# Optimization experiments

Measured on AMD Instinct MI355X. Metric: run time of the kernel, lower is better.

Reference implementation:

```python
import jax, jax.numpy as jnp
import numpy as np

L, B, S, D, H, FF, V, P = 6, 8, 1024, 768, 12, 3072, 50257, 1024
DH = D // H
EPS = 1e-5


def setup_inputs() -> dict:
    key = jax.random.key(0)
    ks = jax.random.split(key, 12)
    std = 0.02
    return {
        "x_ids": jax.random.randint(ks[0], (B, S), 0, V),
        "calibrated_mask": jax.random.normal(ks[1], (B, S, S), jnp.float32),
        "wte": jax.random.normal(ks[2], (V, D), jnp.float32) * std,
        "wpe": jax.random.normal(ks[3], (P, D), jnp.float32) * std,
        "ln1_g": jnp.ones((L, D), jnp.float32),
        "ln1_b": jnp.zeros((L, D), jnp.float32),
        "qkv_w": jax.random.normal(ks[4], (L, D, 3 * D), jnp.float32) * std,
        "qkv_b": jnp.zeros((L, 3 * D), jnp.float32),
        "ao_w": jax.random.normal(ks[5], (L, D, D), jnp.float32) * std,
        "ao_b": jnp.zeros((L, D), jnp.float32),
        "ln2_g": jnp.ones((L, D), jnp.float32),
        "ln2_b": jnp.zeros((L, D), jnp.float32),
        "fc_w": jax.random.normal(ks[6], (L, D, FF), jnp.float32) * std,
        "fc_b": jnp.zeros((L, FF), jnp.float32),
        "op_w": jax.random.normal(ks[7], (L, FF, D), jnp.float32) * std,
        "op_b": jnp.zeros((L, D), jnp.float32),
        "lnf_g": jnp.ones((D,), jnp.float32),
        "lnf_b": jnp.zeros((D,), jnp.float32),
    }


def _ln(x, g, b):
    m = jnp.mean(x, axis=-1, keepdims=True)
    v = jnp.var(x, axis=-1, keepdims=True)
    return (x - m) * jax.lax.rsqrt(v + EPS) * g + b


def _gelu_new(x):
    c = np.sqrt(2.0 / np.pi).astype(np.float32)
    return 0.5 * x * (1.0 + jnp.tanh(c * (x + 0.044715 * x * x * x)))


def _gpt2_forward(x_ids, calibrated_mask, wte, wpe, ln1_g, ln1_b, qkv_w, qkv_b,
                  ao_w, ao_b, ln2_g, ln2_b, fc_w, fc_b, op_w, op_b, lnf_g, lnf_b):
    s = x_ids.shape[1]
    h = wte[x_ids] + wpe[:s][None, :, :]  # [B,S,D]
    causal = jnp.tril(jnp.ones((s, s), bool))
    neg = jnp.finfo(h.dtype).min
    # additive mask, broadcast over heads (unsqueeze(1).repeat over n_head)
    add_mask = calibrated_mask[:, None, :, :]  # [B,1,S,S]

    def block(hid, p):
        l1g, l1b, qw, qb, aw, ab, l2g, l2b, fw, fb, ow, ob = p
        x = _ln(hid, l1g, l1b)
        qkv = x @ qw + qb  # [B,S,3D]
        q, k, v = jnp.split(qkv, 3, axis=-1)
        q = q.reshape(q.shape[0], s, H, DH).transpose(0, 2, 1, 3)
        k = k.reshape(k.shape[0], s, H, DH).transpose(0, 2, 1, 3)
        v = v.reshape(v.shape[0], s, H, DH).transpose(0, 2, 1, 3)
        scores = jnp.einsum('bhqd,bhkd->bhqk', q, k) / jnp.sqrt(jnp.asarray(DH, q.dtype))
        scores = jnp.where(causal[None, None], scores, neg)
        scores = scores + add_mask
        w = jax.nn.softmax(scores, axis=-1)
        a = jnp.einsum('bhqk,bhkd->bhqd', w, v)
        a = a.transpose(0, 2, 1, 3).reshape(a.shape[0], s, D)
        hid = hid + a @ aw + ab
        x2 = _ln(hid, l2g, l2b)
        hid = hid + _gelu_new(x2 @ fw + fb) @ ow + ob
        return hid, None

    params = (ln1_g, ln1_b, qkv_w, qkv_b, ao_w, ao_b, ln2_g, ln2_b, fc_w, fc_b, op_w, op_b)
    h, _ = jax.lax.scan(block, h, params)
    return _ln(h, lnf_g, lnf_b)


def reference(x_ids, calibrated_mask, wte, wpe, ln1_g, ln1_b, qkv_w, qkv_b,
              ao_w, ao_b, ln2_g, ln2_b, fc_w, fc_b, op_w, op_b, lnf_g, lnf_b):
    return _gpt2_forward(x_ids, calibrated_mask, wte, wpe, ln1_g, ln1_b, qkv_w, qkv_b,
                         ao_w, ao_b, ln2_g, ln2_b, fc_w, fc_b, op_w, op_b, lnf_g, lnf_b)
```

## Files before the change

### kernel.cpp

```cpp
#include <hip/hip_runtime.h>
#include <hip/hip_bf16.h>

typedef __bf16 bf16_t;
typedef __bf16 bf16x8 __attribute__((ext_vector_type(8)));
typedef float  f32x4  __attribute__((ext_vector_type(4)));

#define DEV __device__ __forceinline__

DEV void gload_lds16(const void* g, void* l) {
  __builtin_amdgcn_global_load_lds(
      (__attribute__((address_space(1))) void*)(void*)g,
      (__attribute__((address_space(3))) void*)l, 16, 0, 0);
}

__global__ __launch_bounds__(256)
void transpose_cast(const float* __restrict__ in, bf16_t* __restrict__ out,
                    int K, int N) {
  __shared__ float tile[32][33];
  const int k0 = blockIdx.x * 32;
  const int n0 = blockIdx.y * 32;
  const int tx = threadIdx.x;
  const int ty = threadIdx.y;
#pragma unroll
  for (int i = 0; i < 32; i += 8)
    tile[ty + i][tx] = in[(long)(k0 + ty + i) * N + n0 + tx];
  __syncthreads();
#pragma unroll
  for (int i = 0; i < 32; i += 8)
    out[(long)(n0 + ty + i) * K + k0 + tx] = (bf16_t)tile[tx][ty + i];
}

__global__ __launch_bounds__(256)
void embed_kernel(const int* __restrict__ ids, const float* __restrict__ wte,
                  const float* __restrict__ wpe, bf16_t* __restrict__ h) {
  const int idx = blockIdx.x * 256 + threadIdx.x;
  const int col = idx % 768;
  const int row = idx / 768;
  const int s   = row & 1023;
  h[idx] = (bf16_t)(wte[(long)ids[row] * 768 + col] + wpe[s * 768 + col]);
}

template <bool BF16OUT>
__global__ __launch_bounds__(256)
void ln_kernel(const bf16_t* __restrict__ x, const float* __restrict__ g,
               const float* __restrict__ b, bf16_t* __restrict__ ob,
               float* __restrict__ of) {
  const long row = blockIdx.x;
  const bf16_t* xr = x + row * 768;
  const int t = threadIdx.x;
  float v0 = (float)xr[t], v1 = (float)xr[t + 256], v2 = (float)xr[t + 512];
  float s  = v0 + v1 + v2;
  float sq = v0 * v0 + v1 * v1 + v2 * v2;
#pragma unroll
  for (int o = 32; o; o >>= 1) { s += __shfl_down(s, o); sq += __shfl_down(sq, o); }
  __shared__ float red[8];
  const int w = t >> 6;
  if ((t & 63) == 0) { red[w] = s; red[4 + w] = sq; }
  __syncthreads();
  s  = red[0] + red[1] + red[2] + red[3];
  sq = red[4] + red[5] + red[6] + red[7];
  const float mean = s * (1.f / 768.f);
  const float rs = rsqrtf(sq * (1.f / 768.f) - mean * mean + 1e-5f);
  float vv[3] = {v0, v1, v2};
#pragma unroll
  for (int i = 0; i < 3; ++i) {
    const int col = t + i * 256;
    const float o2 = (vv[i] - mean) * rs * g[col] + b[col];
    if (BF16OUT) ob[row * 768 + col] = (bf16_t)o2;
    else         of[row * 768 + col] = o2;
  }
}

template <int EPI, int BN>
__global__ __launch_bounds__(256, 4)
void gemm_bt(const bf16_t* __restrict__ A, const bf16_t* __restrict__ Bt,
             const float* __restrict__ bias, bf16_t* __restrict__ Cb,
             int M, int N, int K) {
  constexpr int NI = BN / 32;
  __shared__ bf16_t As[128 * 64];
  __shared__ bf16_t Bs[BN * 64];
  const int tid  = threadIdx.x;
  const int lane = tid & 63, w = tid >> 6;
  const int col = lane & 15, s16 = lane >> 4;
  const int nbn = N / BN;
  const int cpx = gridDim.x >> 3;
  const int bid = (blockIdx.x & 7) * cpx + (blockIdx.x >> 3);
  const int bm = bid / nbn, bn = bid % nbn;
  const int wr = w >> 1, wc = w & 1;

  f32x4 acc[4][NI];
#pragma unroll
  for (int i = 0; i < 4; ++i)
#pragma unroll
    for (int j = 0; j < NI; ++j) acc[i][j] = f32x4{0.f, 0.f, 0.f, 0.f};

  const long arow0 = (long)bm * 128;
  const long brow0 = (long)bn * BN;

  const int nt = K >> 6;
  for (int t = 0; t < nt; ++t) {
    const int k0 = t << 6;
#pragma unroll
    for (int i = 0; i < 4; ++i) {
      const int c = i * 256 + tid;
      const int row = c >> 3, slot = c & 7;
      gload_lds16(A + (arow0 + row) * (long)K + k0 + ((slot ^ (row & 7)) << 3),
                  (char*)As + c * 16);
    }
#pragma unroll
    for (int i = 0; i < BN / 32; ++i) {
      const int c = i * 256 + tid;
      const int row = c >> 3, slot = c & 7;
      gload_lds16(Bt + (brow0 + row) * (long)K + k0 + ((slot ^ (row & 7)) << 3),
                  (char*)Bs + c * 16);
    }
    __syncthreads();

    bf16x8 af[2][4], bfr[2][NI];
#pragma unroll
    for (int mi = 0; mi < 4; ++mi) {
      const int row = wr * 64 + mi * 16 + col;
#pragma unroll
      for (int ks = 0; ks < 2; ++ks) {
        const int slot = ks * 4 + s16;
        af[ks][mi] = *(const bf16x8*)((char*)As + row * 128 +
                                      ((slot ^ (row & 7)) << 4));
      }
    }
#pragma unroll
    for (int ni = 0; ni < NI; ++ni) {
      const int row = wc * (BN / 2) + ni * 16 + col;
#pragma unroll
      for (int ks = 0; ks < 2; ++ks) {
        const int slot = ks * 4 + s16;
        bfr[ks][ni] = *(const bf16x8*)((char*)Bs + row * 128 +
                                       ((slot ^ (row & 7)) << 4));
      }
    }
#pragma unroll
    for (int ks = 0; ks < 2; ++ks)
#pragma unroll
      for (int mi = 0; mi < 4; ++mi)
#pragma unroll
        for (int ni = 0; ni < NI; ++ni)
          acc[mi][ni] = __builtin_amdgcn_mfma_f32_16x16x32_bf16(
              af[ks][mi], bfr[ks][ni], acc[mi][ni], 0, 0, 0);

    __syncthreads();
  }

  const int colb = bn * BN + wc * (BN / 2) + col;
  const int rowb = bm * 128 + wr * 64 + (s16 << 2);
#pragma unroll
  for (int ni = 0; ni < NI; ++ni) {
    const int ccol = colb + ni * 16;
    const float bv = bias[ccol];
#pragma unroll
    for (int mi = 0; mi < 4; ++mi) {
      const int row = rowb + mi * 16;
#pragma unroll
      for (int r = 0; r < 4; ++r) {
        const float v = acc[mi][ni][r] + bv;
        const long idx = (long)(row + r) * N + ccol;
        if (EPI == 1) {
          Cb[idx] = (bf16_t)((float)Cb[idx] + v);
        } else if (EPI == 2) {
          Cb[idx] = (bf16_t)v;
        } else {
          const float z = 0.7978845608028654f * (v + 0.044715f * v * v * v);
          Cb[idx] = (bf16_t)(v / (1.f + __expf(-2.f * z)));
        }
      }
    }
  }
}

__global__ __launch_bounds__(512, 4)
void gemm_wide(const bf16_t* __restrict__ A, const bf16_t* __restrict__ Bt,
               const float* __restrict__ bias, bf16_t* __restrict__ Cb,
               int M, int N, int K) {
  __shared__ bf16_t As[128 * 64];
  __shared__ bf16_t Bs[256 * 64];
  const int tid = threadIdx.x;
  const int lane = tid & 63, w = tid >> 6;
  const int col = lane & 15, s16 = lane >> 4;
  const int wm = w >> 2, wn = w & 3;
  const int nbn = N >> 8;
  const int cpx = gridDim.x >> 3;
  const int bid = (blockIdx.x & 7) * cpx + (blockIdx.x >> 3);
  const int bm = bid / nbn, bn = bid % nbn;
  const long arow0 = (long)bm * 128, brow0 = (long)bn * 256;

  f32x4 acc[4][4];
#pragma unroll
  for (int i = 0; i < 4; ++i)
#pragma unroll
    for (int j = 0; j < 4; ++j) acc[i][j] = f32x4{0.f, 0.f, 0.f, 0.f};

  const int nt = K >> 6;
  for (int t = 0; t < nt; ++t) {
    const int k0 = t << 6;
#pragma unroll
    for (int i = 0; i < 2; ++i) {
      const int c = i * 512 + tid;
      const int row = c >> 3, slot = c & 7;
      gload_lds16(A + (arow0 + row) * (long)K + k0 + ((slot ^ (row & 7)) << 3),
                  (char*)As + c * 16);
    }
#pragma unroll
    for (int i = 0; i < 4; ++i) {
      const int c = i * 512 + tid;
      const int row = c >> 3, slot = c & 7;
      gload_lds16(Bt + (brow0 + row) * (long)K + k0 + ((slot ^ (row & 7)) << 3),
                  (char*)Bs + c * 16);
    }
    __syncthreads();

    bf16x8 af[2][4], bfr[2][4];
#pragma unroll
    for (int mi = 0; mi < 4; ++mi) {
      const int row = wm * 64 + mi * 16 + col;
#pragma unroll
      for (int ks = 0; ks < 2; ++ks) {
        const int slot = ks * 4 + s16;
        af[ks][mi] = *(const bf16x8*)((char*)As + row * 128 +
                                      ((slot ^ (row & 7)) << 4));
      }
    }
#pragma unroll
    for (int ni = 0; ni < 4; ++ni) {
      const int row = wn * 64 + ni * 16 + col;
#pragma unroll
      for (int ks = 0; ks < 2; ++ks) {
        const int slot = ks * 4 + s16;
        bfr[ks][ni] = *(const bf16x8*)((char*)Bs + row * 128 +
                                       ((slot ^ (row & 7)) << 4));
      }
    }
#pragma unroll
    for (int ks = 0; ks < 2; ++ks)
#pragma unroll
      for (int mi = 0; mi < 4; ++mi)
#pragma unroll
        for (int ni = 0; ni < 4; ++ni)
          acc[mi][ni] = __builtin_amdgcn_mfma_f32_16x16x32_bf16(
              af[ks][mi], bfr[ks][ni], acc[mi][ni], 0, 0, 0);

    __syncthreads();
  }

  const int rowb = bm * 128 + wm * 64 + (s16 << 2);
  const int colb = bn * 256 + wn * 64 + col;
#pragma unroll
  for (int ni = 0; ni < 4; ++ni) {
    const int ccol = colb + ni * 16;
    const float bv = bias[ccol];
#pragma unroll
    for (int mi = 0; mi < 4; ++mi) {
      const int row = rowb + mi * 16;
#pragma unroll
      for (int r = 0; r < 4; ++r)
        Cb[(long)(row + r) * N + ccol] = (bf16_t)(acc[mi][ni][r] + bv);
    }
  }
}

__global__ __launch_bounds__(256, 3)
void attn_kernel(const bf16_t* __restrict__ qkv, const float* __restrict__ mask,
                 bf16_t* __restrict__ out) {
  __shared__ bf16_t Kl[2][64 * 64];
  __shared__ bf16_t Vt[2][64 * 64];
  __shared__ bf16_t Pl[4][16 * 64];
  const int tid = threadIdx.x, lane = tid & 63, w = tid >> 6;
  const int col = lane & 15, s16 = lane >> 4, l7 = lane & 7;
  const int qp = blockIdx.x & 7;
  const int bh = blockIdx.x >> 3;
  const int b = bh / 12, h = bh % 12;
  const int sw0 = (s16 ^ l7) << 4;
  const int sw1 = ((s16 + 4) ^ l7) << 4;
  char* const plw = (char*)&Pl[w][0];
  const long qkvb = (long)b * 1024 * 2304;

  auto stageK = [&](int buf, int k0) {
#pragma unroll
    for (int i = 0; i < 2; ++i) {
      const int c = i * 256 + tid;
      const int krow = c >> 3, slot = c & 7;
      gload_lds16(qkv + qkvb + (long)(k0 + krow) * 2304 + 768 + h * 64 +
                      ((slot ^ (krow & 7)) << 3),
                  (char*)&Kl[buf][0] + i * 4096 + w * 1024);
    }
  };
  auto loadV = [&](int k0, bf16x8& t0, bf16x8& t1) {
    const bf16_t* vbase = qkv + qkvb + 1536 + h * 64;
#pragma unroll
    for (int i = 0; i < 2; ++i) {
      const int c = i * 256 + tid;
      const int d = c & 63, koct = c >> 6;
      const bf16_t* vsrc = vbase + (long)(k0 + koct * 8) * 2304 + d;
      bf16x8 tv;
#pragma unroll
      for (int j = 0; j < 8; ++j) tv[j] = vsrc[(long)j * 2304];
      if (i == 0) t0 = tv; else t1 = tv;
    }
  };
  auto storeV = [&](int buf, const bf16x8& t0, const bf16x8& t1) {
#pragma unroll
    for (int i = 0; i < 2; ++i) {
      const int c = i * 256 + tid;
      const int d = c & 63, koct = c >> 6;
      *(bf16x8*)((char*)&Vt[buf][0] + d * 128 + ((koct ^ (d & 7)) << 4)) =
          (i == 0) ? t0 : t1;
    }
  };

#pragma unroll 1
  for (int pass = 0; pass < 2; ++pass) {
    const int qt = pass ? (15 - qp) : qp;
    const int qrow0 = qt * 64 + w * 16;
    const long rowQ = (long)(b * 1024 + qrow0 + col) * 2304 + h * 64;
    const bf16x8 aq0 = *(const bf16x8*)&qkv[rowQ + s16 * 8];
    const bf16x8 aq1 = *(const bf16x8*)&qkv[rowQ + 32 + s16 * 8];
    const int qb = qrow0 + s16 * 4;
    const float* mrow = mask + ((long)b * 1024 + qb) * 1024;

    auto loadM = [&](int k0, float (&m)[4][4]) {
#pragma unroll
      for (int g = 0; g < 4; ++g)
#pragma unroll
        for (int r = 0; r < 4; ++r)
          m[g][r] = mrow[(long)r * 1024 + k0 + g * 16 + col];
    };

    float m_run[4], l_run[4];
    f32x4 o_acc[4];
#pragma unroll
    for (int r = 0; r < 4; ++r) { m_run[r] = -INFINITY; l_run[r] = 0.f; }
#pragma unroll
    for (int go = 0; go < 4; ++go) o_acc[go] = f32x4{0.f, 0.f, 0.f, 0.f};

    bf16x8 tv0, tv1;
    stageK(0, 0);
    loadV(0, tv0, tv1);
    storeV(0, tv0, tv1);
    float msk[4][4];
    loadM(0, msk);
    __syncthreads();

#pragma unroll 1
    for (int kt = 0; kt <= qt; ++kt) {
      const int cur = kt & 1;
      const bool more = kt < qt;
      const int k0 = kt * 64;
      float mnx[4][4];
      if (more) {
        stageK(cur ^ 1, k0 + 64);
        loadV(k0 + 64, tv0, tv1);
        loadM(k0 + 64, mnx);
      }

      f32x4 sf[4];
      __builtin_amdgcn_s_setprio(1);
#pragma unroll
      for (int g = 0; g < 4; ++g) {
        const int rbyte = (g * 16 + col) * 128;
        bf16x8 bk0 = *(const bf16x8*)((char*)&Kl[cur][0] + rbyte + sw0);
        bf16x8 bk1 = *(const bf16x8*)((char*)&Kl[cur][0] + rbyte + sw1);
        f32x4 z = f32x4{0.f, 0.f, 0.f, 0.f};
        z = __builtin_amdgcn_mfma_f32_16x16x32_bf16(aq0, bk0, z, 0, 0, 0);
        z = __builtin_amdgcn_mfma_f32_16x16x32_bf16(aq1, bk1, z, 0, 0, 0);
        sf[g] = z;
      }
      __builtin_amdgcn_s_setprio(0);

      const bool diag = (kt == qt);
      float sv[4][4];
#pragma unroll
      for (int g = 0; g < 4; ++g)
#pragma unroll
        for (int r = 0; r < 4; ++r) {
          float s = sf[g][r] * 0.125f + msk[g][r];
          if (diag && (k0 + g * 16 + col) > (qb + r)) s = -INFINITY;
          sv[g][r] = s;
        }
#pragma unroll
      for (int r = 0; r < 4; ++r) {
        float mx = fmaxf(fmaxf(sv[0][r], sv[1][r]), fmaxf(sv[2][r], sv[3][r]));
#pragma unroll
        for (int o = 8; o; o >>= 1) mx = fmaxf(mx, __shfl_xor(mx, o));
        const float m_new = fmaxf(m_run[r], mx);
        const float f = __expf(m_run[r] - m_new);
        m_run[r] = m_new;
        float sum = 0.f;
#pragma unroll
        for (int g = 0; g < 4; ++g) {
          const float p = __expf(sv[g][r] - m_new);
          sv[g][r] = p;
          sum += p;
        }
#pragma unroll
        for (int o = 8; o; o >>= 1) sum += __shfl_xor(sum, o);
        l_run[r] = l_run[r] * f + sum;
#pragma unroll
        for (int go = 0; go < 4; ++go) o_acc[go][r] *= f;
      }

#pragma unroll
      for (int g = 0; g < 4; ++g) {
        const int ks = 2 * g + (col >> 3);
#pragma unroll
        for (int r = 0; r < 4; ++r) {
          const int qr = s16 * 4 + r;
          *(bf16_t*)(plw + qr * 128 + ((ks ^ (qr & 7)) << 4) + l7 * 2) = (bf16_t)sv[g][r];
        }
      }
      const bf16x8 pa0 = *(const bf16x8*)(plw + col * 128 + sw0);
      const bf16x8 pa1 = *(const bf16x8*)(plw + col * 128 + sw1);
      __builtin_amdgcn_s_setprio(1);
#pragma unroll
      for (int go = 0; go < 4; ++go) {
        const int dbyte = (go * 16 + col) * 128;
        bf16x8 bv0 = *(const bf16x8*)((char*)&Vt[cur][0] + dbyte + sw0);
        bf16x8 bv1 = *(const bf16x8*)((char*)&Vt[cur][0] + dbyte + sw1);
        o_acc[go] = __builtin_amdgcn_mfma_f32_16x16x32_bf16(pa0, bv0, o_acc[go], 0, 0, 0);
        o_acc[go] = __builtin_amdgcn_mfma_f32_16x16x32_bf16(pa1, bv1, o_acc[go], 0, 0, 0);
      }
      __builtin_amdgcn_s_setprio(0);

      if (more) {
        storeV(cur ^ 1, tv0, tv1);
#pragma unroll
        for (int g = 0; g < 4; ++g)
#pragma unroll
          for (int r = 0; r < 4; ++r) msk[g][r] = mnx[g][r];
      }
      __syncthreads();
    }

    float inv[4];
#pragma unroll
    for (int r = 0; r < 4; ++r) inv[r] = 1.f / l_run[r];
#pragma unroll
    for (int go = 0; go < 4; ++go)
#pragma unroll
      for (int r = 0; r < 4; ++r)
        out[(long)(b * 1024 + qb + r) * 768 + h * 64 + go * 16 + col] =
            (bf16_t)(o_acc[go][r] * inv[r]);
  }
}

extern "C" void kernel_launch(void* const* d_in, const int* in_sizes, int n_in,
                              void* d_out, int out_size, void* d_ws, size_t ws_size,
                              hipStream_t stream) {
  const int*   x_ids = (const int*)d_in[0];
  const float* mask  = (const float*)d_in[1];
  const float* wte   = (const float*)d_in[2];
  const float* wpe   = (const float*)d_in[3];
  const float* ln1_g = (const float*)d_in[4];
  const float* ln1_b = (const float*)d_in[5];
  const float* qkv_w = (const float*)d_in[6];
  const float* qkv_b = (const float*)d_in[7];
  const float* ao_w  = (const float*)d_in[8];
  const float* ao_b  = (const float*)d_in[9];
  const float* ln2_g = (const float*)d_in[10];
  const float* ln2_b = (const float*)d_in[11];
  const float* fc_w  = (const float*)d_in[12];
  const float* fc_b  = (const float*)d_in[13];
  const float* op_w  = (const float*)d_in[14];
  const float* op_b  = (const float*)d_in[15];
  const float* lnf_g = (const float*)d_in[16];
  const float* lnf_b = (const float*)d_in[17];

  char* ws = (char*)d_ws;
  size_t off = 0;
  auto alloc = [&](size_t bytes) {
    char* p = ws + off;
    off += (bytes + 255) & ~(size_t)255;
    return p;
  };
  bf16_t* wqT = (bf16_t*)alloc(6ull * 2304 * 768 * 2);
  bf16_t* waT = (bf16_t*)alloc(6ull * 768 * 768 * 2);
  bf16_t* wfT = (bf16_t*)alloc(6ull * 3072 * 768 * 2);
  bf16_t* woT = (bf16_t*)alloc(6ull * 768 * 3072 * 2);
  bf16_t* h   = (bf16_t*)alloc(8192ull * 768 * 2);
  bf16_t* xb  = (bf16_t*)alloc(8192ull * 768 * 2);
  bf16_t* qkv = (bf16_t*)alloc(8192ull * 2304 * 2);
  bf16_t* abf = (bf16_t*)alloc(8192ull * 768 * 2);
  bf16_t* fb  = (bf16_t*)alloc(8192ull * 3072 * 2);
  if (off > ws_size) return;

  const dim3 tb(32, 8);
  for (int l = 0; l < 6; ++l) {
    transpose_cast<<<dim3(768 / 32, 2304 / 32), tb, 0, stream>>>(
        qkv_w + (long)l * 768 * 2304, wqT + (long)l * 2304 * 768, 768, 2304);
    transpose_cast<<<dim3(768 / 32, 768 / 32), tb, 0, stream>>>(
        ao_w + (long)l * 768 * 768, waT + (long)l * 768 * 768, 768, 768);
    transpose_cast<<<dim3(768 / 32, 3072 / 32), tb, 0, stream>>>(
        fc_w + (long)l * 768 * 3072, wfT + (long)l * 3072 * 768, 768, 3072);
    transpose_cast<<<dim3(3072 / 32, 768 / 32), tb, 0, stream>>>(
        op_w + (long)l * 3072 * 768, woT + (long)l * 768 * 3072, 3072, 768);
  }

  embed_kernel<<<24576, 256, 0, stream>>>(x_ids, wte, wpe, h);

  for (int l = 0; l < 6; ++l) {
    ln_kernel<true><<<8192, 256, 0, stream>>>(h, ln1_g + l * 768, ln1_b + l * 768, xb, nullptr);
    gemm_wide<<<576, 512, 0, stream>>>(xb, wqT + (long)l * 2304 * 768,
                                       qkv_b + l * 2304, qkv, 8192, 2304, 768);
    attn_kernel<<<768, 256, 0, stream>>>(qkv, mask, abf);
    gemm_bt<1, 64><<<768, 256, 0, stream>>>(abf, waT + (long)l * 768 * 768,
                                            ao_b + l * 768, h, 8192, 768, 768);
    ln_kernel<true><<<8192, 256, 0, stream>>>(h, ln2_g + l * 768, ln2_b + l * 768, xb, nullptr);
    gemm_bt<3, 128><<<1536, 256, 0, stream>>>(xb, wfT + (long)l * 3072 * 768,
                                              fc_b + l * 3072, fb, 8192, 3072, 768);
    gemm_bt<1, 64><<<768, 256, 0, stream>>>(fb, woT + (long)l * 768 * 3072,
                                            op_b + l * 768, h, 8192, 768, 3072);
  }

  ln_kernel<false><<<8192, 256, 0, stream>>>(h, lnf_g, lnf_b, nullptr, (float*)d_out);
}
```

Measured before the change: 1.652 ms.

## Batch weight transposes, vectorize embed/LN, retile wide GEMM for QKV and FC

Collapses the 24 per-layer weight transpose launches into 4 launches using a z-grid dimension. Vectorizes the embedding kernel to 8 elements per thread and rewrites layernorm as one wavefront per row with xor-shuffle reduction, removing the shared-memory barrier. Retiles the 512-thread wide GEMM from 128x256 to 256x128 and templates its epilogue so the FC+GELU GEMM also uses it instead of the 256-thread kernel. These target launch overhead, scalar memory traffic and GEMM efficiency, at the risk of different occupancy and tile-quantization behaviour.

```diff
diff --git a/kernel.cpp b/kernel.cpp
--- a/kernel.cpp
+++ b/kernel.cpp
@@ -3,6 +3,7 @@
 
 typedef __bf16 bf16_t;
 typedef __bf16 bf16x8 __attribute__((ext_vector_type(8)));
+typedef __bf16 bf16x4 __attribute__((ext_vector_type(4)));
 typedef float  f32x4  __attribute__((ext_vector_type(4)));
 
 #define DEV __device__ __forceinline__
@@ -17,27 +18,35 @@
 void transpose_cast(const float* __restrict__ in, bf16_t* __restrict__ out,
                     int K, int N) {
   __shared__ float tile[32][33];
+  const long z = blockIdx.z;
+  const float* inz = in + z * (long)K * N;
+  bf16_t* outz = out + z * (long)N * K;
   const int k0 = blockIdx.x * 32;
   const int n0 = blockIdx.y * 32;
   const int tx = threadIdx.x;
   const int ty = threadIdx.y;
 #pragma unroll
   for (int i = 0; i < 32; i += 8)
-    tile[ty + i][tx] = in[(long)(k0 + ty + i) * N + n0 + tx];
+    tile[ty + i][tx] = inz[(long)(k0 + ty + i) * N + n0 + tx];
   __syncthreads();
 #pragma unroll
   for (int i = 0; i < 32; i += 8)
-    out[(long)(n0 + ty + i) * K + k0 + tx] = (bf16_t)tile[tx][ty + i];
+    outz[(long)(n0 + ty + i) * K + k0 + tx] = (bf16_t)tile[tx][ty + i];
 }
 
 __global__ __launch_bounds__(256)
 void embed_kernel(const int* __restrict__ ids, const float* __restrict__ wte,
                   const float* __restrict__ wpe, bf16_t* __restrict__ h) {
-  const int idx = blockIdx.x * 256 + threadIdx.x;
-  const int col = idx % 768;
-  const int row = idx / 768;
+  const int t = blockIdx.x * 256 + threadIdx.x;
+  const int row = t / 96;
+  const int c8  = (t % 96) * 8;
   const int s   = row & 1023;
-  h[idx] = (bf16_t)(wte[(long)ids[row] * 768 + col] + wpe[s * 768 + col]);
+  const float* wr = wte + (long)ids[row] * 768 + c8;
+  const float* pr = wpe + (long)s * 768 + c8;
+  bf16x8 o;
+#pragma unroll
+  for (int j = 0; j < 8; ++j) o[j] = (bf16_t)(wr[j] + pr[j]);
+  *(bf16x8*)&h[(long)row * 768 + c8] = o;
 }
 
 template <bool BF16OUT>
@@ -45,29 +54,48 @@
 void ln_kernel(const bf16_t* __restrict__ x, const float* __restrict__ g,
                const float* __restrict__ b, bf16_t* __restrict__ ob,
                float* __restrict__ of) {
-  const long row = blockIdx.x;
+  const int lane = threadIdx.x & 63;
+  const long row = blockIdx.x * 4 + (threadIdx.x >> 6);
   const bf16_t* xr = x + row * 768;
-  const int t = threadIdx.x;
-  float v0 = (float)xr[t], v1 = (float)xr[t + 256], v2 = (float)xr[t + 512];
-  float s  = v0 + v1 + v2;
-  float sq = v0 * v0 + v1 * v1 + v2 * v2;
-#pragma unroll
-  for (int o = 32; o; o >>= 1) { s += __shfl_down(s, o); sq += __shfl_down(sq, o); }
-  __shared__ float red[8];
-  const int w = t >> 6;
-  if ((t & 63) == 0) { red[w] = s; red[4 + w] = sq; }
-  __syncthreads();
-  s  = red[0] + red[1] + red[2] + red[3];
-  sq = red[4] + red[5] + red[6] + red[7];
+  const bf16x8 v8 = *(const bf16x8*)&xr[lane * 8];
+  const bf16x4 v4 = *(const bf16x4*)&xr[512 + lane * 4];
+  float vv[12];
+#pragma unroll
+  for (int j = 0; j < 8; ++j) vv[j] = (float)v8[j];
+#pragma unroll
+  for (int j = 0; j < 4; ++j) vv[8 + j] = (float)v4[j];
+  float s = 0.f, sq = 0.f;
+#pragma unroll
+  for (int j = 0; j < 12; ++j) { s += vv[j]; sq += vv[j] * vv[j]; }
+#pragma unroll
+  for (int o = 32; o; o >>= 1) { s += __shfl_xor(s, o); sq += __shfl_xor(sq, o); }
   const float mean = s * (1.f / 768.f);
   const float rs = rsqrtf(sq * (1.f / 768.f) - mean * mean + 1e-5f);
-  float vv[3] = {v0, v1, v2};
-#pragma unroll
-  for (int i = 0; i < 3; ++i) {
-    const int col = t + i * 256;
-    const float o2 = (vv[i] - mean) * rs * g[col] + b[col];
-    if (BF16OUT) ob[row * 768 + col] = (bf16_t)o2;
-    else         of[row * 768 + col] = o2;
+  if (BF16OUT) {
+    bf16x8 o8; bf16x4 o4;
+#pragma unroll
+    for (int j = 0; j < 8; ++j) {
+      const int col = lane * 8 + j;
+      o8[j] = (bf16_t)((vv[j] - mean) * rs * g[col] + b[col]);
+    }
+#pragma unroll
+    for (int j = 0; j < 4; ++j) {
+      const int col = 512 + lane * 4 + j;
+      o4[j] = (bf16_t)((vv[8 + j] - mean) * rs * g[col] + b[col]);
+    }
+    *(bf16x8*)&ob[row * 768 + lane * 8] = o8;
+    *(bf16x4*)&ob[row * 768 + 512 + lane * 4] = o4;
+  } else {
+#pragma unroll
+    for (int j = 0; j < 8; ++j) {
+      const int col = lane * 8 + j;
+      of[row * 768 + col] = (vv[j] - mean) * rs * g[col] + b[col];
+    }
+#pragma unroll
+    for (int j = 0; j < 4; ++j) {
+      const int col = 512 + lane * 4 + j;
+      of[row * 768 + col] = (vv[8 + j] - mean) * rs * g[col] + b[col];
+    }
   }
 }
 
@@ -175,21 +203,22 @@
   }
 }
 
+template <int EPI>
 __global__ __launch_bounds__(512, 4)
-void gemm_wide(const bf16_t* __restrict__ A, const bf16_t* __restrict__ Bt,
-               const float* __restrict__ bias, bf16_t* __restrict__ Cb,
-               int M, int N, int K) {
-  __shared__ bf16_t As[128 * 64];
-  __shared__ bf16_t Bs[256 * 64];
+void gemm_bw(const bf16_t* __restrict__ A, const bf16_t* __restrict__ Bt,
+             const float* __restrict__ bias, bf16_t* __restrict__ Cb,
+             int M, int N, int K) {
+  __shared__ bf16_t As[256 * 64];
+  __shared__ bf16_t Bs[128 * 64];
   const int tid = threadIdx.x;
   const int lane = tid & 63, w = tid >> 6;
   const int col = lane & 15, s16 = lane >> 4;
-  const int wm = w >> 2, wn = w & 3;
-  const int nbn = N >> 8;
+  const int wm = w >> 1, wn = w & 1;
+  const int nbn = N >> 7;
   const int cpx = gridDim.x >> 3;
   const int bid = (blockIdx.x & 7) * cpx + (blockIdx.x >> 3);
   const int bm = bid / nbn, bn = bid % nbn;
-  const long arow0 = (long)bm * 128, brow0 = (long)bn * 256;
+  const long arow0 = (long)bm * 256, brow0 = (long)bn * 128;
 
   f32x4 acc[4][4];
 #pragma unroll
@@ -201,14 +230,14 @@
   for (int t = 0; t < nt; ++t) {
     const int k0 = t << 6;
 #pragma unroll
-    for (int i = 0; i < 2; ++i) {
+    for (int i = 0; i < 4; ++i) {
       const int c = i * 512 + tid;
       const int row = c >> 3, slot = c & 7;
       gload_lds16(A + (arow0 + row) * (long)K + k0 + ((slot ^ (row & 7)) << 3),
                   (char*)As + c * 16);
     }
 #pragma unroll
-    for (int i = 0; i < 4; ++i) {
+    for (int i = 0; i < 2; ++i) {
       const int c = i * 512 + tid;
       const int row = c >> 3, slot = c & 7;
       gload_lds16(Bt + (brow0 + row) * (long)K + k0 + ((slot ^ (row & 7)) << 3),
@@ -249,8 +278,8 @@
     __syncthreads();
   }
 
-  const int rowb = bm * 128 + wm * 64 + (s16 << 2);
-  const int colb = bn * 256 + wn * 64 + col;
+  const int rowb = bm * 256 + wm * 64 + (s16 << 2);
+  const int colb = bn * 128 + wn * 64 + col;
 #pragma unroll
   for (int ni = 0; ni < 4; ++ni) {
     const int ccol = colb + ni * 16;
@@ -259,8 +288,14 @@
     for (int mi = 0; mi < 4; ++mi) {
       const int row = rowb + mi * 16;
 #pragma unroll
-      for (int r = 0; r < 4; ++r)
-        Cb[(long)(row + r) * N + ccol] = (bf16_t)(acc[mi][ni][r] + bv);
+      for (int r = 0; r < 4; ++r) {
+        const float v = acc[mi][ni][r] + bv;
+        if (EPI == 2) Cb[(long)(row + r) * N + ccol] = (bf16_t)v;
+        else {
+          const float z = 0.7978845608028654f * (v + 0.044715f * v * v * v);
+          Cb[(long)(row + r) * N + ccol] = (bf16_t)(v / (1.f + __expf(-2.f * z)));
+        }
+      }
     }
   }
 }
@@ -490,32 +525,26 @@
   if (off > ws_size) return;
 
   const dim3 tb(32, 8);
+  transpose_cast<<<dim3(768 / 32, 2304 / 32, 6), tb, 0, stream>>>(qkv_w, wqT, 768, 2304);
+  transpose_cast<<<dim3(768 / 32, 768 / 32, 6), tb, 0, stream>>>(ao_w, waT, 768, 768);
+  transpose_cast<<<dim3(768 / 32, 3072 / 32, 6), tb, 0, stream>>>(fc_w, wfT, 768, 3072);
+  transpose_cast<<<dim3(3072 / 32, 768 / 32, 6), tb, 0, stream>>>(op_w, woT, 3072, 768);
+
+  embed_kernel<<<3072, 256, 0, stream>>>(x_ids, wte, wpe, h);
+
   for (int l = 0; l < 6; ++l) {
-    transpose_cast<<<dim3(768 / 32, 2304 / 32), tb, 0, stream>>>(
-        qkv_w + (long)l * 768 * 2304, wqT + (long)l * 2304 * 768, 768, 2304);
-    transpose_cast<<<dim3(768 / 32, 768 / 32), tb, 0, stream>>>(
-        ao_w + (long)l * 768 * 768, waT + (long)l * 768 * 768, 768, 768);
-    transpose_cast<<<dim3(768 / 32, 3072 / 32), tb, 0, stream>>>(
-        fc_w + (long)l * 768 * 3072, wfT + (long)l * 3072 * 768, 768, 3072);
-    transpose_cast<<<dim3(3072 / 32, 768 / 32), tb, 0, stream>>>(
-        op_w + (long)l * 3072 * 768, woT + (long)l * 768 * 3072, 3072, 768);
-  }
-
-  embed_kernel<<<24576, 256, 0, stream>>>(x_ids, wte, wpe, h);
-
-  for (int l = 0; l < 6; ++l) {
-    ln_kernel<true><<<8192, 256, 0, stream>>>(h, ln1_g + l * 768, ln1_b + l * 768, xb, nullptr);
-    gemm_wide<<<576, 512, 0, stream>>>(xb, wqT + (long)l * 2304 * 768,
-                                       qkv_b + l * 2304, qkv, 8192, 2304, 768);
+    ln_kernel<true><<<2048, 256, 0, stream>>>(h, ln1_g + l * 768, ln1_b + l * 768, xb, nullptr);
+    gemm_bw<2><<<576, 512, 0, stream>>>(xb, wqT + (long)l * 2304 * 768,
+                                        qkv_b + l * 2304, qkv, 8192, 2304, 768);
     attn_kernel<<<768, 256, 0, stream>>>(qkv, mask, abf);
     gemm_bt<1, 64><<<768, 256, 0, stream>>>(abf, waT + (long)l * 768 * 768,
                                             ao_b + l * 768, h, 8192, 768, 768);
-    ln_kernel<true><<<8192, 256, 0, stream>>>(h, ln2_g + l * 768, ln2_b + l * 768, xb, nullptr);
-    gemm_bt<3, 128><<<1536, 256, 0, stream>>>(xb, wfT + (long)l * 3072 * 768,
-                                              fc_b + l * 3072, fb, 8192, 3072, 768);
+    ln_kernel<true><<<2048, 256, 0, stream>>>(h, ln2_g + l * 768, ln2_b + l * 768, xb, nullptr);
+    gemm_bw<3><<<768, 512, 0, stream>>>(xb, wfT + (long)l * 3072 * 768,
+                                        fc_b + l * 3072, fb, 8192, 3072, 768);
     gemm_bt<1, 64><<<768, 256, 0, stream>>>(fb, woT + (long)l * 768 * 3072,
                                             op_b + l * 768, h, 8192, 768, 3072);
   }
 
-  ln_kernel<false><<<8192, 256, 0, stream>>>(h, lnf_g, lnf_b, nullptr, (float*)d_out);
-}
+  ln_kernel<false><<<2048, 256, 0, stream>>>(h, lnf_g, lnf_b, nullptr, (float*)d_out);
+}
```

Measured after the change: 1.600 ms. -3.2%, faster.
